# Performance work log

Hardware: AMD Instinct MI355X
Metric: run time of the kernel (lower is better)

Reference implementation:

```python
import jax, jax.numpy as jnp
import numpy as np

D_MODEL = 1024
C_OUT = 64
PRED_LEN = 96
D_STATE = 64
D_CONV = 4
EXPAND = 2
D_INNER = EXPAND * D_MODEL          # 2048
DT_RANK = D_MODEL // 16             # 64
IN_DIM = D_MODEL + C_OUT
BATCH = 512


def setup_inputs() -> dict:
    key = jax.random.key(0)
    ks = jax.random.split(key, 10)
    def w(k, shape, scale=0.02):
        return jax.random.normal(k, shape, dtype=jnp.float32) * scale
    return {
        "context": jax.random.normal(ks[0], (BATCH, D_MODEL), dtype=jnp.float32),
        "initial_values": jax.random.normal(ks[1], (BATCH, C_OUT), dtype=jnp.float32),
        "w_in": w(ks[2], (IN_DIM, 2 * D_INNER)),
        "b_in": jnp.zeros((2 * D_INNER,), jnp.float32),
        "conv_w": w(ks[3], (D_INNER, D_CONV)),
        "conv_b": jnp.zeros((D_INNER,), jnp.float32),
        "w_x": w(ks[4], (D_INNER, DT_RANK + 2 * D_STATE)),
        "w_dt": w(ks[5], (DT_RANK, D_INNER)),
        "b_dt": jnp.zeros((D_INNER,), jnp.float32),
        "A_log": jnp.log(jnp.broadcast_to(jnp.arange(1, D_STATE + 1, dtype=jnp.float32), (D_INNER, D_STATE))),
        "D_skip": jnp.ones((D_INNER,), jnp.float32),
        "w_out": w(ks[6], (D_INNER, D_MODEL)),
        "b_out": jnp.zeros((D_MODEL,), jnp.float32),
        "w_proj": w(ks[7], (D_MODEL, C_OUT)),
        "b_proj": jnp.zeros((C_OUT,), jnp.float32),
    }


def _mamba_len1(u, w_in, b_in, conv_w, conv_b, w_x, w_dt, b_dt, D_skip, w_out, b_out):
    """Standard Mamba block applied to a length-1 sequence (fresh state each call,
    matching the torch module, which calls mamba on [B,1,D] every step).
    With h0 = 0 and L = 1, the exp(dt*A) recurrence term vanishes, so A_log has no effect."""
    xz = u @ w_in + b_in                         # [B, 2*D_INNER]
    x, z = jnp.split(xz, 2, axis=-1)             # [B, D_INNER] each
    # causal depthwise conv over L=1: only the last kernel tap hits the current input
    x = x * conv_w[:, -1] + conv_b
    x = jax.nn.silu(x)
    xdbc = x @ w_x                               # [B, DT_RANK + 2*D_STATE]
    dt = jax.nn.softplus(xdbc[:, :DT_RANK] @ w_dt + b_dt)          # [B, D_INNER]
    Bm = xdbc[:, DT_RANK:DT_RANK + D_STATE]                         # [B, D_STATE]
    Cm = xdbc[:, DT_RANK + D_STATE:]                                # [B, D_STATE]
    # h = (dt*x)[:, :, None] * Bm[:, None, :]; y = sum_s h * Cm  ->  factored form
    y = (dt * x) * jnp.sum(Bm * Cm, axis=-1, keepdims=True)         # [B, D_INNER]
    y = y + D_skip * x
    y = y * jax.nn.silu(z)
    return y @ w_out + b_out                     # [B, D_MODEL]


def reference(context, initial_values, w_in, b_in, conv_w, conv_b, w_x, w_dt,
              b_dt, A_log, D_skip, w_out, b_out, w_proj, b_proj):
    del A_log  # no effect with fresh zero SSM state and seq_len=1 (see _mamba_len1)

    def step(prev_pred, _):
        u = jnp.concatenate([context, prev_pred], axis=-1)          # [B, IN_DIM]
        h = _mamba_len1(u, w_in, b_in, conv_w, conv_b, w_x, w_dt, b_dt,
                        D_skip, w_out, b_out)                        # [B, D_MODEL]
        pred = h @ w_proj + b_proj                                   # [B, C_OUT]
        return pred, pred

    _, preds = jax.lax.scan(step, initial_values, None, length=PRED_LEN)
    return jnp.transpose(preds, (1, 0, 2))       # [B, PRED_LEN, C_OUT]
```

## Files before the change

kernel.cpp:

```cpp
#include <hip/hip_runtime.h>
#include <math.h>


typedef __fp16 half2_t __attribute__((ext_vector_type(2)));
typedef unsigned int uint32;
union HU { uint32 u; half2_t h; };

__device__ __forceinline__ float sigf(float v){
  return __builtin_amdgcn_rcpf(1.f + __expf(-v));
}
__device__ __forceinline__ uint32 pk2(float a, float b){
  HU x; x.h = __builtin_amdgcn_cvt_pkrtz(a, b); return x.u;
}
__device__ __forceinline__ float dot2(uint32 a, uint32 b, float c){
  HU ua, ub; ua.u = a; ub.u = b;
  return __builtin_amdgcn_fdot2(ua.h, ub.h, c, false);
}


__global__ __launch_bounds__(256) void k_ctx(
    const float* __restrict__ ctxin, const float* __restrict__ w_in,
    const float* __restrict__ b_in, float* __restrict__ ctx_xz){
  int tid = threadIdx.x;
  int j = blockIdx.x*256 + tid;
  int b0 = blockIdx.y*16;
  const float* cp = ctxin + (size_t)b0*1024;
  float acc[16];
#pragma unroll
  for (int r=0;r<16;r++) acc[r]=0.f;
  for (int k=0;k<1024;k+=4){
    float w0 = w_in[(size_t)(k+0)*4096 + j];
    float w1 = w_in[(size_t)(k+1)*4096 + j];
    float w2 = w_in[(size_t)(k+2)*4096 + j];
    float w3 = w_in[(size_t)(k+3)*4096 + j];
#pragma unroll
    for (int r=0;r<16;r++){
      acc[r] += cp[r*1024+k]*w0 + cp[r*1024+k+1]*w1
              + cp[r*1024+k+2]*w2 + cp[r*1024+k+3]*w3;
    }
  }
  float bj = b_in[j];
#pragma unroll
  for (int r=0;r<16;r++) ctx_xz[(size_t)(b0+r)*4096 + j] = acc[r] + bj;
}

__global__ __launch_bounds__(256) void k_wop(
    const float* __restrict__ w_out, const float* __restrict__ w_proj,
    const float* __restrict__ b_out, const float* __restrict__ b_proj,
    float* __restrict__ W_op, float* __restrict__ b_op){
  int g = blockIdx.x, tid = threadIdx.x;
  if (g == 512){
    if (tid < 64){
      float s = b_proj[tid];
      for (int k=0;k<1024;k++) s += b_out[k]*w_proj[k*64+tid];
      b_op[tid] = s;
    }
    return;
  }
  int idx = g*256 + tid;
  int c = idx>>6, o = idx&63;
  float s = 0.f;
  const float* wr = w_out + (size_t)c*1024;
  for (int k=0;k<1024;k++) s += wr[k]*w_proj[k*64+o];
  W_op[idx] = s;
}

__global__ __launch_bounds__(256) void k_cvec(
    const float* __restrict__ b_op, const float* __restrict__ w_in2,
    float* __restrict__ cvec){
  int j = blockIdx.x*256 + threadIdx.x;
  float s = 0.f;
  for (int o=0;o<64;o++) s += b_op[o]*w_in2[(size_t)o*4096 + j];
  cvec[j] = s;
}

__global__ __launch_bounds__(256) void k_pack(
    const float* __restrict__ src, uint32* __restrict__ dst,
    int inner, int total){
  int idx = blockIdx.x*256 + threadIdx.x;
  if (idx >= total) return;
  int p = idx / inner, i = idx - p*inner;
  dst[idx] = pk2(src[(size_t)(2*p)*inner + i], src[(size_t)(2*p+1)*inner + i]);
}

__global__ __launch_bounds__(256) void k_pack_wx(
    const float* __restrict__ w_x, uint32* __restrict__ dst){
  int idx = blockIdx.x*256 + threadIdx.x;
  int q = idx & 3;
  int t = idx >> 2;
  int n = t % 192;
  int g = t / 192;
  int k2 = g*4 + q;
  dst[idx] = pk2(w_x[(size_t)(2*k2)*192 + n], w_x[(size_t)(2*k2+1)*192 + n]);
}

__global__ __launch_bounds__(256) void k_pack_wop(
    const float* __restrict__ W_op, uint32* __restrict__ dst){
  int idx = blockIdx.x*256 + threadIdx.x;
  int q = idx & 3;
  int t = idx >> 2;
  int o = t & 63;
  int g = t >> 6;
  int k2 = g*4 + q;
  dst[idx] = pk2(W_op[(size_t)(2*k2)*64 + o], W_op[(size_t)(2*k2+1)*64 + o]);
}

__global__ __launch_bounds__(256) void k_pack_wdt(
    const float* __restrict__ w_dt, uint32* __restrict__ dst){
  int idx = blockIdx.x*256 + threadIdx.x;
  int e = idx & 3;
  int t = idx >> 2;
  int c2 = t & 1023;
  int jp = t >> 10;
  int p = jp*2 + (e>>1);
  int c = c2*2 + (e&1);
  dst[idx] = pk2(w_dt[(size_t)(2*p)*2048 + c], w_dt[(size_t)(2*p+1)*2048 + c]);
}


__global__ __launch_bounds__(1024,4) void k_steps(
    const float* __restrict__ ctx_xz, const float* __restrict__ cvec,
    const uint32* __restrict__ h_in2p, const float* __restrict__ conv_w,
    const float* __restrict__ conv_b,  const uint32* __restrict__ wxp4,
    const uint32* __restrict__ wdtp4,  const float* __restrict__ b_dt,
    const float* __restrict__ D_skip,  const uint32* __restrict__ wopp4,
    const float* __restrict__ b_op,    const float* __restrict__ initial,
    float* __restrict__ dout)
{
  const int tid = threadIdx.x;
  const int r0  = blockIdx.x * 2;

  __shared__ uint2  predH2[32];
  __shared__ __align__(16) uint32 xbufH[2][1024];
  __shared__ float  zbuf[2][2048];
  __shared__ uint4  xdh2q[16];
  __shared__ float  bcL[2];
  __shared__ float  pxd[4][384];
  __shared__ float  ppd[16][130];

  const int cb = tid*4;
  const bool isx = (cb < 2048);
  float4 cw4, cb4;
  if (isx){
    cw4 = make_float4(conv_w[(cb+0)*4+3], conv_w[(cb+1)*4+3],
                      conv_w[(cb+2)*4+3], conv_w[(cb+3)*4+3]);
    cb4 = *(const float4*)&conv_b[cb];
  }
  const float4 cv4   = *(const float4*)&cvec[cb];
  const float4 ctxr0 = *(const float4*)&ctx_xz[(size_t)(r0+0)*4096 + cb];
  const float4 ctxr1 = *(const float4*)&ctx_xz[(size_t)(r0+1)*4096 + cb];
  const int c2t = tid*2;
  const float2 bdt2 = *(const float2*)&b_dt[c2t];
  const float2 dsk2 = *(const float2*)&D_skip[c2t];
  const int n2  = tid % 192;
  const int ks2 = tid / 192;
  const int o4  = tid & 63;
  const int kb2 = (tid >> 6) * 64;
  const float bopv = b_op[(tid>>1) & 63];

  uint4 wop[16];
  {
    const uint4* wo4 = (const uint4*)wopp4 + (size_t)(tid>>6)*1024 + o4;
#pragma unroll
    for (int j=0;j<16;j++) wop[j] = wo4[(size_t)j*64];
  }

  if (tid < 128){
    float v = initial[(size_t)(r0 + (tid&1))*64 + (tid>>1)];
    float vp = __shfl_down(v, 2, 64);
    if ((tid & 2) == 0)
      ((uint32*)predH2)[(tid>>2)*2 + (tid&1)] = pk2(v, vp);
  }
  __syncthreads();

  for (int t=0; t<96; t++){
    const float tf = (t > 0) ? 1.f : 0.f;
    float a0[4], a1[4];
#pragma unroll
    for (int i=0;i<4;i++){
      float c = (&cv4.x)[i];
      a0[i] = (&ctxr0.x)[i] + tf*c;
      a1[i] = (&ctxr1.x)[i] + tf*c;
    }
    {
      const uint32* wp = h_in2p + cb;
#pragma unroll 8
      for (int o2=0;o2<32;o2++){
        uint4 w  = *(const uint4*)&wp[(size_t)o2*4096];
        uint2 pd = *((const uint2*)predH2 + o2);
        a0[0]=dot2(w.x,pd.x,a0[0]); a0[1]=dot2(w.y,pd.x,a0[1]);
        a0[2]=dot2(w.z,pd.x,a0[2]); a0[3]=dot2(w.w,pd.x,a0[3]);
        a1[0]=dot2(w.x,pd.y,a1[0]); a1[1]=dot2(w.y,pd.y,a1[1]);
        a1[2]=dot2(w.z,pd.y,a1[2]); a1[3]=dot2(w.w,pd.y,a1[3]);
      }
    }
    if (isx){
      float x0[4], x1[4];
#pragma unroll
      for (int i=0;i<4;i++){
        float v0 = a0[i]*(&cw4.x)[i] + (&cb4.x)[i];
        float v1 = a1[i]*(&cw4.x)[i] + (&cb4.x)[i];
        x0[i] = v0*sigf(v0);
        x1[i] = v1*sigf(v1);
      }
      const int p = cb >> 1;
      *(uint2*)&xbufH[0][p] = make_uint2(pk2(x0[0], x0[1]), pk2(x0[2], x0[3]));
      *(uint2*)&xbufH[1][p] = make_uint2(pk2(x1[0], x1[1]), pk2(x1[2], x1[3]));
    } else {
      float4 z0, z1;
#pragma unroll
      for (int i=0;i<4;i++){
        (&z0.x)[i] = a0[i]*sigf(a0[i]);
        (&z1.x)[i] = a1[i]*sigf(a1[i]);
      }
      *(float4*)&zbuf[0][cb-2048] = z0;
      *(float4*)&zbuf[1][cb-2048] = z1;
    }
    __syncthreads();

    if (tid < 768){
      const uint4* wp4 = (const uint4*)wxp4 + (size_t)ks2*12288 + n2;
      const uint4* xb0 = (const uint4*)&xbufH[0][ks2*256];
      const uint4* xb1 = (const uint4*)&xbufH[1][ks2*256];
      float f0 = 0.f, f1 = 0.f;
#pragma unroll 8
      for (int j=0;j<64;j++){
        uint4 w  = wp4[(size_t)j*192];
        uint4 x0 = xb0[j];
        uint4 x1 = xb1[j];
        f0 = dot2(w.x, x0.x, f0); f1 = dot2(w.x, x1.x, f1);
        f0 = dot2(w.y, x0.y, f0); f1 = dot2(w.y, x1.y, f1);
        f0 = dot2(w.z, x0.z, f0); f1 = dot2(w.z, x1.z, f1);
        f0 = dot2(w.w, x0.w, f0); f1 = dot2(w.w, x1.w, f1);
      }
      *(float2*)&pxd[ks2][n2*2] = make_float2(f0, f1);
    }
    __syncthreads();

    if (tid < 128){
      int r = tid >> 6, nl = tid & 63;
      int ib = (64+nl)*2 + r, ic = (128+nl)*2 + r;
      float bv = pxd[0][ib] + pxd[1][ib] + pxd[2][ib] + pxd[3][ib];
      float cv = pxd[0][ic] + pxd[1][ic] + pxd[2][ic] + pxd[3][ic];
      float p = bv * cv;
#pragma unroll
      for (int sh=1; sh<64; sh<<=1) p += __shfl_xor(p, sh, 64);
      if (nl == 0) bcL[r] = p;
    } else if (tid < 160){
      int o2 = tid - 128;
      int i00 = (2*o2)*2, i10 = (2*o2+1)*2;
      float v00 = pxd[0][i00  ] + pxd[1][i00  ] + pxd[2][i00  ] + pxd[3][i00  ];
      float v01 = pxd[0][i00+1] + pxd[1][i00+1] + pxd[2][i00+1] + pxd[3][i00+1];
      float v10 = pxd[0][i10  ] + pxd[1][i10  ] + pxd[2][i10  ] + pxd[3][i10  ];
      float v11 = pxd[0][i10+1] + pxd[1][i10+1] + pxd[2][i10+1] + pxd[3][i10+1];
      ((uint32*)xdh2q)[o2*2+0] = pk2(v00, v10);
      ((uint32*)xdh2q)[o2*2+1] = pk2(v01, v11);
    }
    __syncthreads();

    float d00=0.f, d01=0.f, d10=0.f, d11=0.f;
    {
      const uint4* wd4 = (const uint4*)wdtp4 + tid;
#pragma unroll 8
      for (int jp=0;jp<16;jp++){
        uint4 w  = wd4[(size_t)jp*1024];
        uint4 xd = xdh2q[jp];
        d00 = dot2(w.x, xd.x, d00);
        d01 = dot2(w.y, xd.x, d01);
        d10 = dot2(w.x, xd.y, d10);
        d11 = dot2(w.y, xd.y, d11);
        d00 = dot2(w.z, xd.z, d00);
        d01 = dot2(w.w, xd.z, d01);
        d10 = dot2(w.z, xd.w, d10);
        d11 = dot2(w.w, xd.w, d11);
      }
    }
    {
      float bc0 = bcL[0], bc1 = bcL[1];
      HU xh0, xh1; xh0.u = xbufH[0][tid]; xh1.u = xbufH[1][tid];
      float2 zr0 = *(const float2*)&zbuf[0][c2t];
      float2 zr1 = *(const float2*)&zbuf[1][c2t];
      float v00 = d00 + bdt2.x, v01 = d01 + bdt2.y;
      float v10 = d10 + bdt2.x, v11 = d11 + bdt2.y;
      float s00 = (v00 > 15.f) ? v00 : __logf(1.f + __expf(v00));
      float s01 = (v01 > 15.f) ? v01 : __logf(1.f + __expf(v01));
      float s10 = (v10 > 15.f) ? v10 : __logf(1.f + __expf(v10));
      float s11 = (v11 > 15.f) ? v11 : __logf(1.f + __expf(v11));
      float y00 = (s00*bc0 + dsk2.x) * (float)xh0.h.x * zr0.x;
      float y01 = (s01*bc0 + dsk2.y) * (float)xh0.h.y * zr0.y;
      float y10 = (s10*bc1 + dsk2.x) * (float)xh1.h.x * zr1.x;
      float y11 = (s11*bc1 + dsk2.y) * (float)xh1.h.y * zr1.y;
      xbufH[0][tid] = pk2(y00, y01);
      xbufH[1][tid] = pk2(y10, y11);
    }
    __syncthreads();

    {
      const uint4* yb0 = (const uint4*)&xbufH[0][kb2];
      const uint4* yb1 = (const uint4*)&xbufH[1][kb2];
      float p0 = 0.f, p1 = 0.f;
#pragma unroll
      for (int j=0;j<16;j++){
        uint4 w  = wop[j];
        uint4 y0 = yb0[j];
        uint4 y1 = yb1[j];
        p0 = dot2(w.x, y0.x, p0); p1 = dot2(w.x, y1.x, p1);
        p0 = dot2(w.y, y0.y, p0); p1 = dot2(w.y, y1.y, p1);
        p0 = dot2(w.z, y0.z, p0); p1 = dot2(w.z, y1.z, p1);
        p0 = dot2(w.w, y0.w, p0); p1 = dot2(w.w, y1.w, p1);
      }
      *(float2*)&ppd[tid>>6][o4*2] = make_float2(p0, p1);
    }
    __syncthreads();

    if (tid < 128){
      float v = 0.f;
#pragma unroll
      for (int ks=0; ks<16; ks++) v += ppd[ks][tid];
      int o = tid >> 1, r = tid & 1;
      dout[((size_t)(r0+r)*96 + t)*64 + o] = v + bopv;
      float vp = __shfl_down(v, 2, 64);
      if ((tid & 2) == 0)
        ((uint32*)predH2)[(tid>>2)*2 + (tid&1)] = pk2(v, vp);
    }
    __syncthreads();
  }
}


extern "C" void kernel_launch(void* const* d_in, const int* in_sizes, int n_in,
                              void* d_out, int out_size, void* d_ws, size_t ws_size,
                              hipStream_t stream)
{
  const float* context = (const float*)d_in[0];
  const float* initial = (const float*)d_in[1];
  const float* w_in    = (const float*)d_in[2];
  const float* b_in    = (const float*)d_in[3];
  const float* conv_w  = (const float*)d_in[4];
  const float* conv_b  = (const float*)d_in[5];
  const float* w_x     = (const float*)d_in[6];
  const float* w_dt    = (const float*)d_in[7];
  const float* b_dt    = (const float*)d_in[8];
  const float* D_skip  = (const float*)d_in[10];
  const float* w_out   = (const float*)d_in[11];
  const float* b_out   = (const float*)d_in[12];
  const float* w_proj  = (const float*)d_in[13];
  const float* b_proj  = (const float*)d_in[14];

  float* ws = (float*)d_ws;
  float*  ctx_xz = ws;
  float*  cvec   = ctx_xz + 2097152;
  float*  W_op   = cvec + 4096;
  float*  b_op   = W_op + 131072;
  uint32* h_in2p = (uint32*)(b_op + 128);
  uint32* wxp4   = h_in2p + 131072;
  uint32* wdtp4  = wxp4 + 196608;
  uint32* wopp4  = wdtp4 + 65536;
  float*  dout   = (float*)d_out;

  const float* w_in2 = w_in + (size_t)1024*4096;

  k_wop     <<<dim3(513),   256, 0, stream>>>(w_out, w_proj, b_out, b_proj, W_op, b_op);
  k_cvec    <<<dim3(16),    256, 0, stream>>>(b_op, w_in2, cvec);
  k_ctx     <<<dim3(16,32), 256, 0, stream>>>(context, w_in, b_in, ctx_xz);
  k_pack    <<<dim3(512),   256, 0, stream>>>(w_in2, h_in2p, 4096, 131072);
  k_pack_wx <<<dim3(768),   256, 0, stream>>>(w_x,  wxp4);
  k_pack_wdt<<<dim3(256),   256, 0, stream>>>(w_dt, wdtp4);
  k_pack_wop<<<dim3(256),   256, 0, stream>>>(W_op, wopp4);

  k_steps<<<dim3(256), 1024, 0, stream>>>(ctx_xz, cvec, h_in2p, conv_w, conv_b,
                                          wxp4, wdtp4, b_dt, D_skip, wopp4, b_op,
                                          initial, dout);
}
```

Baseline: 2.209 ms.

## Prefetch next stage's weights into registers across barriers in step loop

Before each barrier, every thread now issues register loads for the first eight weight chunks of the next matmul stage (in_proj, x_proj, dt_proj, out_proj), so global-memory latency overlaps the barrier wait and the preceding compute. The out_proj weights are no longer held resident in registers for the whole loop; only half are prefetched each step and the rest are reloaded. The pxd shared array is padded to reduce bank conflicts. This trades register pressure and extra weight reloads for hidden latency at synchronisation points.

Result: slower. 5.229 ms (+136.6%).

```diff
diff --git a/kernel.cpp b/kernel.cpp
--- a/kernel.cpp
+++ b/kernel.cpp
@@ -135,7 +135,7 @@
   __shared__ float  zbuf[2][2048];
   __shared__ uint4  xdh2q[16];
   __shared__ float  bcL[2];
-  __shared__ float  pxd[4][384];
+  __shared__ float  pxd[4][388];
   __shared__ float  ppd[16][130];
 
   const int cb = tid*4;
@@ -158,12 +158,14 @@
   const int kb2 = (tid >> 6) * 64;
   const float bopv = b_op[(tid>>1) & 63];
 
-  uint4 wop[16];
-  {
-    const uint4* wo4 = (const uint4*)wopp4 + (size_t)(tid>>6)*1024 + o4;
-#pragma unroll
-    for (int j=0;j<16;j++) wop[j] = wo4[(size_t)j*64];
-  }
+  const uint32* wp1 = h_in2p + cb;
+  const uint4*  wp4 = (const uint4*)wxp4 + (size_t)ks2*12288 + n2;
+  const uint4*  wd4 = (const uint4*)wdtp4 + tid;
+  const uint4*  wo4 = (const uint4*)wopp4 + (size_t)(tid>>6)*1024 + o4;
+
+  uint4 pf1[8];
+#pragma unroll
+  for (int o2=0;o2<8;o2++) pf1[o2] = *(const uint4*)&wp1[(size_t)o2*4096];
 
   if (tid < 128){
     float v = initial[(size_t)(r0 + (tid&1))*64 + (tid>>1)];
@@ -183,16 +185,24 @@
       a1[i] = (&ctxr1.x)[i] + tf*c;
     }
     {
-      const uint32* wp = h_in2p + cb;
-#pragma unroll 8
-      for (int o2=0;o2<32;o2++){
-        uint4 w  = *(const uint4*)&wp[(size_t)o2*4096];
+#pragma unroll
+      for (int o2=0;o2<8;o2++){
+        uint4 w  = pf1[o2];
         uint2 pd = *((const uint2*)predH2 + o2);
         a0[0]=dot2(w.x,pd.x,a0[0]); a0[1]=dot2(w.y,pd.x,a0[1]);
         a0[2]=dot2(w.z,pd.x,a0[2]); a0[3]=dot2(w.w,pd.x,a0[3]);
         a1[0]=dot2(w.x,pd.y,a1[0]); a1[1]=dot2(w.y,pd.y,a1[1]);
         a1[2]=dot2(w.z,pd.y,a1[2]); a1[3]=dot2(w.w,pd.y,a1[3]);
       }
+#pragma unroll 8
+      for (int o2=8;o2<32;o2++){
+        uint4 w  = *(const uint4*)&wp1[(size_t)o2*4096];
+        uint2 pd = *((const uint2*)predH2 + o2);
+        a0[0]=dot2(w.x,pd.x,a0[0]); a0[1]=dot2(w.y,pd.x,a0[1]);
+        a0[2]=dot2(w.z,pd.x,a0[2]); a0[3]=dot2(w.w,pd.x,a0[3]);
+        a1[0]=dot2(w.x,pd.y,a1[0]); a1[1]=dot2(w.y,pd.y,a1[1]);
+        a1[2]=dot2(w.z,pd.y,a1[2]); a1[3]=dot2(w.w,pd.y,a1[3]);
+      }
     }
     if (isx){
       float x0[4], x1[4];
@@ -216,15 +226,30 @@
       *(float4*)&zbuf[0][cb-2048] = z0;
       *(float4*)&zbuf[1][cb-2048] = z1;
     }
-    __syncthreads();
-
+    uint4 pf2[8];
     if (tid < 768){
-      const uint4* wp4 = (const uint4*)wxp4 + (size_t)ks2*12288 + n2;
+#pragma unroll
+      for (int j=0;j<8;j++) pf2[j] = wp4[(size_t)j*192];
+    }
+    __syncthreads();
+
+    uint4 pfd[8];
+    if (tid < 768){
       const uint4* xb0 = (const uint4*)&xbufH[0][ks2*256];
       const uint4* xb1 = (const uint4*)&xbufH[1][ks2*256];
       float f0 = 0.f, f1 = 0.f;
+#pragma unroll
+      for (int j=0;j<8;j++){
+        uint4 w  = pf2[j];
+        uint4 x0 = xb0[j];
+        uint4 x1 = xb1[j];
+        f0 = dot2(w.x, x0.x, f0); f1 = dot2(w.x, x1.x, f1);
+        f0 = dot2(w.y, x0.y, f0); f1 = dot2(w.y, x1.y, f1);
+        f0 = dot2(w.z, x0.z, f0); f1 = dot2(w.z, x1.z, f1);
+        f0 = dot2(w.w, x0.w, f0); f1 = dot2(w.w, x1.w, f1);
+      }
 #pragma unroll 8
-      for (int j=0;j<64;j++){
+      for (int j=8;j<64;j++){
         uint4 w  = wp4[(size_t)j*192];
         uint4 x0 = xb0[j];
         uint4 x1 = xb1[j];
@@ -235,6 +260,8 @@
       }
       *(float2*)&pxd[ks2][n2*2] = make_float2(f0, f1);
     }
+#pragma unroll
+    for (int jp=0;jp<8;jp++) pfd[jp] = wd4[(size_t)jp*1024];
     __syncthreads();
 
     if (tid < 128){
@@ -260,9 +287,21 @@
 
     float d00=0.f, d01=0.f, d10=0.f, d11=0.f;
     {
-      const uint4* wd4 = (const uint4*)wdtp4 + tid;
-#pragma unroll 8
-      for (int jp=0;jp<16;jp++){
+#pragma unroll
+      for (int jp=0;jp<8;jp++){
+        uint4 w  = pfd[jp];
+        uint4 xd = xdh2q[jp];
+        d00 = dot2(w.x, xd.x, d00);
+        d01 = dot2(w.y, xd.x, d01);
+        d10 = dot2(w.x, xd.y, d10);
+        d11 = dot2(w.y, xd.y, d11);
+        d00 = dot2(w.z, xd.z, d00);
+        d01 = dot2(w.w, xd.z, d01);
+        d10 = dot2(w.z, xd.w, d10);
+        d11 = dot2(w.w, xd.w, d11);
+      }
+#pragma unroll
+      for (int jp=8;jp<16;jp++){
         uint4 w  = wd4[(size_t)jp*1024];
         uint4 xd = xdh2q[jp];
         d00 = dot2(w.x, xd.x, d00);
@@ -275,6 +314,9 @@
         d11 = dot2(w.w, xd.w, d11);
       }
     }
+    uint4 pfo[8];
+#pragma unroll
+    for (int j=0;j<8;j++) pfo[j] = wo4[(size_t)j*64];
     {
       float bc0 = bcL[0], bc1 = bcL[1];
       HU xh0, xh1; xh0.u = xbufH[0][tid]; xh1.u = xbufH[1][tid];
@@ -300,8 +342,8 @@
       const uint4* yb1 = (const uint4*)&xbufH[1][kb2];
       float p0 = 0.f, p1 = 0.f;
 #pragma unroll
-      for (int j=0;j<16;j++){
-        uint4 w  = wop[j];
+      for (int j=0;j<8;j++){
+        uint4 w  = pfo[j];
         uint4 y0 = yb0[j];
         uint4 y1 = yb1[j];
         p0 = dot2(w.x, y0.x, p0); p1 = dot2(w.x, y1.x, p1);
@@ -309,8 +351,20 @@
         p0 = dot2(w.z, y0.z, p0); p1 = dot2(w.z, y1.z, p1);
         p0 = dot2(w.w, y0.w, p0); p1 = dot2(w.w, y1.w, p1);
       }
+#pragma unroll
+      for (int j=8;j<16;j++){
+        uint4 w  = wo4[(size_t)j*64];
+        uint4 y0 = yb0[j];
+        uint4 y1 = yb1[j];
+        p0 = dot2(w.x, y0.x, p0); p1 = dot2(w.x, y1.x, p1);
+        p0 = dot2(w.y, y0.y, p0); p1 = dot2(w.y, y1.y, p1);
+        p0 = dot2(w.z, y0.z, p0); p1 = dot2(w.z, y1.z, p1);
+        p0 = dot2(w.w, y0.w, p0); p1 = dot2(w.w, y1.w, p1);
+      }
       *(float2*)&ppd[tid>>6][o4*2] = make_float2(p0, p1);
     }
+#pragma unroll
+    for (int o2=0;o2<8;o2++) pf1[o2] = *(const uint4*)&wp1[(size_t)o2*4096];
     __syncthreads();
 
     if (tid < 128){
```

## Stage dt-projection weights into LDS via async loads; stream output weights from global

Applied to the files above, without the earlier changes.

Idle threads (tid>=768) issue global_load_lds copies of the first 7 of 16 w_dt chunks into a new 112KB shared buffer while the x_proj GEMV runs, and the dt GEMV then reads those chunks from LDS. The per-thread register cache of w_out weights is dropped and those weights are reloaded from global memory each step, freeing registers. The pxd array is also padded. The intent is to overlap weight fetch with compute and to ease register pressure, at the cost of a much larger LDS footprint and extra global traffic for w_out.

Result: slower. 2.329 ms (+5.4%).

```diff
diff --git a/kernel.cpp b/kernel.cpp
--- a/kernel.cpp
+++ b/kernel.cpp
@@ -15,6 +15,11 @@
 __device__ __forceinline__ float dot2(uint32 a, uint32 b, float c){
   HU ua, ub; ua.u = a; ub.u = b;
   return __builtin_amdgcn_fdot2(ua.h, ub.h, c, false);
+}
+__device__ __forceinline__ void stage16(const uint4* g, uint4* l){
+  __builtin_amdgcn_global_load_lds(
+      (const __attribute__((address_space(1))) void*)g,
+      (__attribute__((address_space(3))) void*)l, 16, 0, 0);
 }
 
 
@@ -135,8 +140,9 @@
   __shared__ float  zbuf[2][2048];
   __shared__ uint4  xdh2q[16];
   __shared__ float  bcL[2];
-  __shared__ float  pxd[4][384];
+  __shared__ float  pxd[4][388];
   __shared__ float  ppd[16][130];
+  __shared__ uint4  sbD[7168];
 
   const int cb = tid*4;
   const bool isx = (cb < 2048);
@@ -158,12 +164,8 @@
   const int kb2 = (tid >> 6) * 64;
   const float bopv = b_op[(tid>>1) & 63];
 
-  uint4 wop[16];
-  {
-    const uint4* wo4 = (const uint4*)wopp4 + (size_t)(tid>>6)*1024 + o4;
-#pragma unroll
-    for (int j=0;j<16;j++) wop[j] = wo4[(size_t)j*64];
-  }
+  const uint4* wdq = (const uint4*)wdtp4;
+  const uint32* wp1 = h_in2p + cb;
 
   if (tid < 128){
     float v = initial[(size_t)(r0 + (tid&1))*64 + (tid>>1)];
@@ -183,10 +185,9 @@
       a1[i] = (&ctxr1.x)[i] + tf*c;
     }
     {
-      const uint32* wp = h_in2p + cb;
 #pragma unroll 8
       for (int o2=0;o2<32;o2++){
-        uint4 w  = *(const uint4*)&wp[(size_t)o2*4096];
+        uint4 w  = *(const uint4*)&wp1[(size_t)o2*4096];
         uint2 pd = *((const uint2*)predH2 + o2);
         a0[0]=dot2(w.x,pd.x,a0[0]); a0[1]=dot2(w.y,pd.x,a0[1]);
         a0[2]=dot2(w.z,pd.x,a0[2]); a0[3]=dot2(w.w,pd.x,a0[3]);
@@ -234,6 +235,13 @@
         f0 = dot2(w.w, x0.w, f0); f1 = dot2(w.w, x1.w, f1);
       }
       *(float2*)&pxd[ks2][n2*2] = make_float2(f0, f1);
+    } else {
+      const int pi = tid - 768;
+#pragma unroll
+      for (int k=0;k<28;k++){
+        int idx = k*256 + pi;
+        stage16(wdq + idx, &sbD[idx]);
+      }
     }
     __syncthreads();
 
@@ -260,10 +268,22 @@
 
     float d00=0.f, d01=0.f, d10=0.f, d11=0.f;
     {
-      const uint4* wd4 = (const uint4*)wdtp4 + tid;
-#pragma unroll 8
-      for (int jp=0;jp<16;jp++){
-        uint4 w  = wd4[(size_t)jp*1024];
+#pragma unroll
+      for (int jp=0;jp<7;jp++){
+        uint4 w  = sbD[jp*1024 + tid];
+        uint4 xd = xdh2q[jp];
+        d00 = dot2(w.x, xd.x, d00);
+        d01 = dot2(w.y, xd.x, d01);
+        d10 = dot2(w.x, xd.y, d10);
+        d11 = dot2(w.y, xd.y, d11);
+        d00 = dot2(w.z, xd.z, d00);
+        d01 = dot2(w.w, xd.z, d01);
+        d10 = dot2(w.z, xd.w, d10);
+        d11 = dot2(w.w, xd.w, d11);
+      }
+#pragma unroll
+      for (int jp=7;jp<16;jp++){
+        uint4 w  = wdq[(size_t)jp*1024 + tid];
         uint4 xd = xdh2q[jp];
         d00 = dot2(w.x, xd.x, d00);
         d01 = dot2(w.y, xd.x, d01);
@@ -296,12 +316,13 @@
     __syncthreads();
 
     {
+      const uint4* wo4 = (const uint4*)wopp4 + (size_t)(tid>>6)*1024 + o4;
       const uint4* yb0 = (const uint4*)&xbufH[0][kb2];
       const uint4* yb1 = (const uint4*)&xbufH[1][kb2];
       float p0 = 0.f, p1 = 0.f;
-#pragma unroll
+#pragma unroll 8
       for (int j=0;j<16;j++){
-        uint4 w  = wop[j];
+        uint4 w  = wo4[(size_t)j*64];
         uint4 y0 = yb0[j];
         uint4 y1 = yb1[j];
         p0 = dot2(w.x, y0.x, p0); p1 = dot2(w.x, y1.x, p1);
```
